# Performance work log

Measured on AMD Instinct MI355X. Metric: run time of the kernel, lower is better.

Reference implementation:

```python
import jax, jax.numpy as jnp
import numpy as np

B, S, D, H, DFF = 2, 2048, 1024, 16, 4096
DK = D // H
EPS = 1e-6

def setup_inputs() -> dict:
    key = jax.random.key(0)
    ks = jax.random.split(key, 12)
    sc = 0.02
    inp = {
        "x": jax.random.normal(ks[0], (B, S, D), jnp.float32),
        "src_mask": jax.random.randint(ks[1], (B, 1, 1, S), 0, 2, jnp.int32),
        "wq": jax.random.normal(ks[2], (D, D), jnp.float32) * sc,
        "bq": jnp.zeros((D,), jnp.float32),
        "wk": jax.random.normal(ks[3], (D, D), jnp.float32) * sc,
        "bk": jnp.zeros((D,), jnp.float32),
        "wv": jax.random.normal(ks[4], (D, D), jnp.float32) * sc,
        "bv": jnp.zeros((D,), jnp.float32),
        "wo": jax.random.normal(ks[5], (D, D), jnp.float32) * sc,
        "bo": jnp.zeros((D,), jnp.float32),
        "w1": jax.random.normal(ks[6], (DFF, D), jnp.float32) * sc,
        "b1": jnp.zeros((DFF,), jnp.float32),
        "w2": jax.random.normal(ks[7], (D, DFF), jnp.float32) * sc,
        "b2": jnp.zeros((D,), jnp.float32),
        "a1": jnp.ones((1,), jnp.float32),
        "be1": jnp.zeros((1,), jnp.float32),
        "a2": jnp.ones((1,), jnp.float32),
        "be2": jnp.zeros((1,), jnp.float32),
    }
    return inp

def layer_norm(x, alpha, beta):
    # custom LN: unbiased std (ddof=1), scalar alpha/beta, divide by (std + eps)
    mean = jnp.mean(x, axis=-1, keepdims=True)
    std = jnp.std(x, axis=-1, keepdims=True, ddof=1)
    return alpha * (x - mean) / (std + EPS) + beta

def mha(x, mask, wq, bq, wk, bk, wv, bv, wo, bo):
    q = (x @ wq.T + bq).reshape(B, S, H, DK).transpose(0, 2, 1, 3)  # [B,H,S,DK]
    k = (x @ wk.T + bk).reshape(B, S, H, DK).transpose(0, 2, 1, 3)
    v = (x @ wv.T + bv).reshape(B, S, H, DK).transpose(0, 2, 1, 3)
    scores = jnp.einsum('bhqd,bhkd->bhqk', q, k) / jnp.sqrt(jnp.float32(DK))
    scores = jnp.where(mask == 0, jnp.float32(-1e9), scores)
    attn = jax.nn.softmax(scores, axis=-1)
    out = jnp.einsum('bhqk,bhkd->bhqd', attn, v)
    out = out.transpose(0, 2, 1, 3).reshape(B, S, D)
    return out @ wo.T + bo

def ffn(x, w1, b1, w2, b2):
    h = jax.nn.relu(x @ w1.T + b1)
    return h @ w2.T + b2

def reference(x, src_mask, wq, bq, wk, bk, wv, bv, wo, bo, w1, b1, w2, b2, a1, be1, a2, be2):
    # pre-norm residual 1: self-attention
    x = x + mha(layer_norm(x, a1, be1), src_mask, wq, bq, wk, bk, wv, bv, wo, bo)
    # pre-norm residual 2: FFN
    x = x + ffn(layer_norm(x, a2, be2), w1, b1, w2, b2)
    return x
```

## Files before the change

### kernel.cpp

```cpp
#include <hip/hip_runtime.h>

#define B_    2
#define S_    2048
#define D_    1024
#define H_    16
#define DK_   64
#define DFF_  4096
#define MROWS (B_*S_)

typedef float f32x4 __attribute__((ext_vector_type(4)));
typedef __bf16 bf16x8 __attribute__((ext_vector_type(8)));

static __device__ __forceinline__ unsigned short f2bf(float f) {
    union { __bf16 h; unsigned short u; } cv;
    cv.h = (__bf16)f;
    return cv.u;
}

static __device__ __forceinline__ void gload16(const unsigned short* g, unsigned short* l) {
    __builtin_amdgcn_global_load_lds((const __attribute__((address_space(1))) void*)g,
                                     (__attribute__((address_space(3))) void*)l, 16, 0, 0);
}

__global__ __launch_bounds__(256) void prep_kernel(
    const float* __restrict__ wq, const float* __restrict__ wk,
    const float* __restrict__ wv, const float* __restrict__ wo,
    const float* __restrict__ w1, const float* __restrict__ w2,
    const float* __restrict__ bq, const float* __restrict__ bk,
    unsigned short* __restrict__ wqkb, unsigned short* __restrict__ wvb,
    unsigned short* __restrict__ wob, unsigned short* __restrict__ w1b,
    unsigned short* __restrict__ w2b, float* __restrict__ bqk) {
    int blk = blockIdx.x;
    if (blk >= 12288) {
        int t0 = threadIdx.x * 8;
        #pragma unroll
        for (int i = 0; i < 8; i++) {
            int j = t0 + i;
            bqk[j] = (j < 1024) ? bq[j] : bk[j - 1024];
        }
        return;
    }
    const float* src; unsigned short* dst; int lb;
    if      (blk < 1024) { src = wq; dst = wqkb;             lb = blk;        }
    else if (blk < 2048) { src = wk; dst = wqkb + (1 << 20); lb = blk - 1024; }
    else if (blk < 3072) { src = wv; dst = wvb;              lb = blk - 2048; }
    else if (blk < 4096) { src = wo; dst = wob;              lb = blk - 3072; }
    else if (blk < 8192) { src = w1; dst = w1b;              lb = blk - 4096; }
    else                 { src = w2; dst = w2b;              lb = blk - 8192; }
    int i4 = lb * 256 + threadIdx.x;
    float4 v = ((const float4*)src)[i4];
    ushort4 o;
    o.x = f2bf(v.x); o.y = f2bf(v.y); o.z = f2bf(v.z); o.w = f2bf(v.w);
    ((ushort4*)dst)[i4] = o;
}

__global__ __launch_bounds__(256) void ln_kernel(const float* __restrict__ x,
                                                 const float* __restrict__ alphap,
                                                 const float* __restrict__ betap,
                                                 unsigned short* __restrict__ out) {
    int row = blockIdx.x;
    int t = threadIdx.x;
    const float* xr = x + (size_t)row * D_;
    float4 v = ((const float4*)xr)[t];
    float s  = v.x + v.y + v.z + v.w;
    float s2 = v.x*v.x + v.y*v.y + v.z*v.z + v.w*v.w;
    #pragma unroll
    for (int o = 1; o < 64; o <<= 1) { s += __shfl_xor(s, o); s2 += __shfl_xor(s2, o); }
    __shared__ float ss[4], ss2[4];
    if ((t & 63) == 0) { ss[t >> 6] = s; ss2[t >> 6] = s2; }
    __syncthreads();
    float S  = ss[0] + ss[1] + ss[2] + ss[3];
    float S2 = ss2[0] + ss2[1] + ss2[2] + ss2[3];
    float mean = S * (1.f / (float)D_);
    float var  = (S2 - S * mean) / (float)(D_ - 1);
    float alpha = alphap[0], beta = betap[0];
    float inv = alpha / (sqrtf(fmaxf(var, 0.f)) + 1e-6f);
    ushort4 o4;
    o4.x = f2bf((v.x - mean) * inv + beta);
    o4.y = f2bf((v.y - mean) * inv + beta);
    o4.z = f2bf((v.z - mean) * inv + beta);
    o4.w = f2bf((v.w - mean) * inv + beta);
    ((ushort4*)(out + (size_t)row * D_))[t] = o4;
}

template<int BN, int EPI, int BIAS_ROW, int QSCALE>
__global__ __launch_bounds__(256) void gemm_bt(const unsigned short* __restrict__ A,
                                               const unsigned short* __restrict__ W,
                                               const float* __restrict__ bias,
                                               const float* __restrict__ resid,
                                               unsigned short* __restrict__ outb,
                                               float* __restrict__ outf,
                                               int M, int N, int K) {
    constexpr int NI = BN / 32;
    __shared__ __align__(16) unsigned short As[128 * 64];
    __shared__ __align__(16) unsigned short Bs[BN * 64];
    const int t = threadIdx.x, lane = t & 63, w = t >> 6;
    const int nwg  = gridDim.x * gridDim.y;
    const int orig = blockIdx.y * gridDim.x + blockIdx.x;
    const int wg   = (orig & 7) * (nwg >> 3) + (orig >> 3);
    const int bx   = wg % gridDim.x, by = wg / gridDim.x;
    const int m0 = by * 128, n0 = bx * BN;
    const int wm = (w & 1) * 64;
    const int wn = (BN == 128) ? (w >> 1) * 64 : (w >> 1) * 32;
    const int l15 = lane & 15, l4 = lane >> 4;
    const int ar0 = w * 8 + (lane >> 3);
    const int ac0 = (lane & 7) * 8;

    f32x4 acc[4][NI];
    f32x4 z4 = {0.f, 0.f, 0.f, 0.f};
    #pragma unroll
    for (int i = 0; i < 4; i++)
        #pragma unroll
        for (int j = 0; j < NI; j++) acc[i][j] = z4;

    const unsigned short* Ap = A + (size_t)m0 * K;
    const unsigned short* Wp = W + (size_t)n0 * K;

    for (int k0 = 0; k0 < K; k0 += 64) {
        #pragma unroll
        for (int j = 0; j < 4; j++)
            gload16(Ap + (size_t)(j*32 + ar0) * K + k0 + ac0, &As[(j*4 + w) * 512]);
        #pragma unroll
        for (int j = 0; j < BN/32; j++)
            gload16(Wp + (size_t)(j*32 + ar0) * K + k0 + ac0, &Bs[(j*4 + w) * 512]);
        __syncthreads();

        #pragma unroll
        for (int ks = 0; ks < 2; ks++) {
            bf16x8 af[4], bfr[NI];
            #pragma unroll
            for (int mi = 0; mi < 4; mi++)
                af[mi] = *(const bf16x8*)&As[(wm + mi*16 + l15)*64 + ks*32 + l4*8];
            #pragma unroll
            for (int ni = 0; ni < NI; ni++)
                bfr[ni] = *(const bf16x8*)&Bs[(wn + ni*16 + l15)*64 + ks*32 + l4*8];
            #pragma unroll
            for (int mi = 0; mi < 4; mi++)
                #pragma unroll
                for (int ni = 0; ni < NI; ni++)
                    acc[mi][ni] = __builtin_amdgcn_mfma_f32_16x16x32_bf16(af[mi], bfr[ni], acc[mi][ni], 0, 0, 0);
        }
        __syncthreads();
    }

    #pragma unroll
    for (int mi = 0; mi < 4; mi++) {
        #pragma unroll
        for (int ni = 0; ni < NI; ni++) {
            int gc = n0 + wn + ni*16 + l15;
            float bc = BIAS_ROW ? 0.f : bias[gc];
            #pragma unroll
            for (int j = 0; j < 4; j++) {
                int gr = m0 + wm + mi*16 + 4*l4 + j;
                float val = acc[mi][ni][j] + (BIAS_ROW ? bias[gr] : bc);
                if (EPI == 1) val = fmaxf(val, 0.f);
                if (QSCALE) { if (gc < (N >> 1)) val *= 0.125f; }
                if (EPI == 2) {
                    val += resid[(size_t)gr * N + gc];
                    outf[(size_t)gr * N + gc] = val;
                } else {
                    outb[(size_t)gr * N + gc] = f2bf(val);
                }
            }
        }
    }
}

__global__ __launch_bounds__(256) void attn_kernel(const unsigned short* __restrict__ qk,
                                                   const unsigned short* __restrict__ vt,
                                                   const int* __restrict__ mask,
                                                   unsigned short* __restrict__ out) {
    __shared__ __align__(16) unsigned short Ks[64*64], Vs[64*64], Ps[64*64];
    __shared__ float mF[64];
    const int t = threadIdx.x, lane = t & 63, w = t >> 6;
    const int l15 = lane & 15, l4 = lane >> 4;
    const int bh = blockIdx.y, b = bh >> 4, h = bh & 15;
    const int q0 = blockIdx.x * 64;
    const unsigned short* qb  = qk + ((size_t)(b * S_ + q0)) * 2048 + h * DK_;
    const unsigned short* kb  = qk + ((size_t)(b * S_)) * 2048 + 1024 + h * DK_;
    const unsigned short* vtb = vt + (size_t)(h * DK_) * MROWS + (size_t)b * S_;

    bf16x8 aq[2];
    #pragma unroll
    for (int ks = 0; ks < 2; ks++)
        aq[ks] = *(const bf16x8*)(qb + (size_t)(w*16 + l15) * 2048 + ks*32 + l4*8);

    float m_ = -INFINITY, l_ = 0.f;
    f32x4 accd[4];
    f32x4 z4 = {0.f, 0.f, 0.f, 0.f};
    #pragma unroll
    for (int dt = 0; dt < 4; dt++) accd[dt] = z4;

    const int r_  = t >> 3, c8_ = (t & 7) * 8;
    const int cs_ = c8_ ^ ((r_ & 7) << 3);
    const int rsw = (l15 & 7) << 3;

    for (int kv0 = 0; kv0 < S_; kv0 += 64) {
        #pragma unroll
        for (int p2 = 0; p2 < 2; p2++) {
            int r = r_ + p2 * 32;
            *(uint4*)&Ks[r*64 + cs_] = *(const uint4*)(kb  + (size_t)(kv0 + r) * 2048 + c8_);
            *(uint4*)&Vs[r*64 + cs_] = *(const uint4*)(vtb + (size_t)r * MROWS + kv0 + c8_);
        }
        if (t < 64) mF[t] = (mask[(size_t)b * S_ + kv0 + t] == 0) ? -1e9f : 0.f;
        __syncthreads();

        f32x4 sc[4];
        #pragma unroll
        for (int nt = 0; nt < 4; nt++) sc[nt] = z4;
        #pragma unroll
        for (int nt = 0; nt < 4; nt++)
            #pragma unroll
            for (int ks = 0; ks < 2; ks++) {
                bf16x8 kf = *(const bf16x8*)&Ks[(nt*16 + l15)*64 + ((ks*32 + 8*l4) ^ rsw)];
                sc[nt] = __builtin_amdgcn_mfma_f32_16x16x32_bf16(kf, aq[ks], sc[nt], 0, 0, 0);
            }

        float sv[4][4];
        #pragma unroll
        for (int nt = 0; nt < 4; nt++) {
            float4 ma = *(const float4*)&mF[nt*16 + 4*l4];
            sv[nt][0] = sc[nt][0] + ma.x;
            sv[nt][1] = sc[nt][1] + ma.y;
            sv[nt][2] = sc[nt][2] + ma.z;
            sv[nt][3] = sc[nt][3] + ma.w;
        }

        float mt = fmaxf(fmaxf(fmaxf(sv[0][0], sv[0][1]), fmaxf(sv[0][2], sv[0][3])),
                         fmaxf(fmaxf(sv[1][0], sv[1][1]), fmaxf(sv[1][2], sv[1][3])));
        mt = fmaxf(mt, fmaxf(fmaxf(fmaxf(sv[2][0], sv[2][1]), fmaxf(sv[2][2], sv[2][3])),
                             fmaxf(fmaxf(sv[3][0], sv[3][1]), fmaxf(sv[3][2], sv[3][3]))));
        mt = fmaxf(mt, __shfl_xor(mt, 16));
        mt = fmaxf(mt, __shfl_xor(mt, 32));

        if (__any(mt > m_)) {
            float mn  = fmaxf(m_, mt);
            float esc = __expf(m_ - mn);
            m_ = mn;
            l_ *= esc;
            float ea[4];
            #pragma unroll
            for (int j = 0; j < 4; j++) ea[j] = __shfl(esc, 4*l4 + j);
            #pragma unroll
            for (int dt = 0; dt < 4; dt++)
                #pragma unroll
                for (int j = 0; j < 4; j++) accd[dt][j] *= ea[j];
        }

        float p[4][4];
        float rsum = 0.f;
        #pragma unroll
        for (int nt = 0; nt < 4; nt++)
            #pragma unroll
            for (int j = 0; j < 4; j++) { p[nt][j] = __expf(sv[nt][j] - m_); rsum += p[nt][j]; }
        rsum += __shfl_xor(rsum, 16);
        rsum += __shfl_xor(rsum, 32);
        l_ += rsum;

        #pragma unroll
        for (int nt = 0; nt < 4; nt++) {
            uint2 w2;
            w2.x = (unsigned)f2bf(p[nt][0]) | ((unsigned)f2bf(p[nt][1]) << 16);
            w2.y = (unsigned)f2bf(p[nt][2]) | ((unsigned)f2bf(p[nt][3]) << 16);
            int key0 = nt*16 + 4*l4;
            *(uint2*)&Ps[(w*16 + l15)*64 + (key0 ^ rsw)] = w2;
        }

        bf16x8 pa[2];
        #pragma unroll
        for (int ks = 0; ks < 2; ks++)
            pa[ks] = *(const bf16x8*)&Ps[(w*16 + l15)*64 + ((ks*32 + 8*l4) ^ rsw)];
        #pragma unroll
        for (int dt = 0; dt < 4; dt++)
            #pragma unroll
            for (int ks = 0; ks < 2; ks++) {
                bf16x8 vv8 = *(const bf16x8*)&Vs[(dt*16 + l15)*64 + ((ks*32 + 8*l4) ^ rsw)];
                accd[dt] = __builtin_amdgcn_mfma_f32_16x16x32_bf16(pa[ks], vv8, accd[dt], 0, 0, 0);
            }
        __syncthreads();
    }

    float inv = 1.f / l_;
    float ia[4];
    #pragma unroll
    for (int j = 0; j < 4; j++) ia[j] = __shfl(inv, 4*l4 + j);
    unsigned short* ob = out + ((size_t)(b * S_ + q0)) * D_ + h * DK_;
    #pragma unroll
    for (int j = 0; j < 4; j++) {
        int r = w*16 + 4*l4 + j;
        #pragma unroll
        for (int dt = 0; dt < 4; dt++)
            ob[(size_t)r * D_ + dt*16 + l15] = f2bf(accd[dt][j] * ia[j]);
    }
}

extern "C" void kernel_launch(void* const* d_in, const int* in_sizes, int n_in,
                              void* d_out, int out_size, void* d_ws, size_t ws_size,
                              hipStream_t stream) {
    const float* x    = (const float*)d_in[0];
    const int*   mask = (const int*)d_in[1];
    const float* wq = (const float*)d_in[2];
    const float* bq = (const float*)d_in[3];
    const float* wk = (const float*)d_in[4];
    const float* bk = (const float*)d_in[5];
    const float* wv = (const float*)d_in[6];
    const float* bv = (const float*)d_in[7];
    const float* wo = (const float*)d_in[8];
    const float* bo = (const float*)d_in[9];
    const float* w1 = (const float*)d_in[10];
    const float* b1 = (const float*)d_in[11];
    const float* w2 = (const float*)d_in[12];
    const float* b2 = (const float*)d_in[13];
    const float* a1  = (const float*)d_in[14];
    const float* be1 = (const float*)d_in[15];
    const float* a2  = (const float*)d_in[16];
    const float* be2 = (const float*)d_in[17];
    float* out = (float*)d_out;

    char* ws = (char*)d_ws;
    unsigned short* wqkb = (unsigned short*)(ws + (0ull  << 20));
    unsigned short* wvb  = (unsigned short*)(ws + (4ull  << 20));
    unsigned short* wob  = (unsigned short*)(ws + (6ull  << 20));
    unsigned short* w1b  = (unsigned short*)(ws + (8ull  << 20));
    unsigned short* w2b  = (unsigned short*)(ws + (16ull << 20));
    unsigned short* xn   = (unsigned short*)(ws + (24ull << 20));
    unsigned short* qkb  = (unsigned short*)(ws + (32ull << 20));
    unsigned short* vtb  = (unsigned short*)(ws + (48ull << 20));
    float*          bqk  = (float*)         (ws + (60ull << 20));
    unsigned short* hh   = qkb;
    float*          x1   = (float*)(ws + (64ull << 20));

    dim3 blk(256);

    prep_kernel<<<12289, blk, 0, stream>>>(wq, wk, wv, wo, w1, w2, bq, bk,
                                           wqkb, wvb, wob, w1b, w2b, bqk);

    ln_kernel<<<MROWS, blk, 0, stream>>>(x, a1, be1, xn);

    dim3 gqk(2048/128, MROWS/128);
    gemm_bt<128,0,0,1><<<gqk, blk, 0, stream>>>(xn, wqkb, bqk, nullptr, qkb, nullptr, MROWS, 2048, D_);

    dim3 gvt(MROWS/64, D_/128);
    gemm_bt<64,0,1,0><<<gvt, blk, 0, stream>>>(wvb, xn, bv, nullptr, vtb, nullptr, D_, MROWS, D_);

    dim3 ga(S_/64, B_*H_);
    attn_kernel<<<ga, blk, 0, stream>>>(qkb, vtb, mask, xn);

    dim3 go(D_/64, MROWS/128);
    gemm_bt<64,2,0,0><<<go, blk, 0, stream>>>(xn, wob, bo, x, nullptr, x1, MROWS, D_, D_);

    ln_kernel<<<MROWS, blk, 0, stream>>>(x1, a2, be2, xn);

    dim3 gf1(DFF_/128, MROWS/128);
    gemm_bt<128,1,0,0><<<gf1, blk, 0, stream>>>(xn, w1b, b1, nullptr, hh, nullptr, MROWS, DFF_, D_);

    gemm_bt<64,2,0,0><<<go, blk, 0, stream>>>(hh, w2b, b2, x1, nullptr, out, MROWS, D_, DFF_);
}
```

Measured before the change: 417.0 us.

## Merge QKV GEMMs, add double-buffered 256x256 FFN1 GEMM, use exp2 softmax

Several changes land together. The QK and V-transposed projections are merged into one launch that splits its blocks between the two GEMMs, which removes one launch and lets the two overlap. FFN1 now runs on a new 256x256-tile, 512-thread GEMM with double-buffered LDS, XOR-swizzled shared memory and setprio around MFMA bursts, which raises data reuse and overlaps the next tile's global loads with compute. The attention softmax switches to exp2 by folding log2(e) into the Q scale (0.125*1.4427). The big tile uses 128KB of LDS, so occupancy drops to one block per CU, and the FFN1 grid is now only 256 workgroups.

```diff
diff --git a/kernel.cpp b/kernel.cpp
--- a/kernel.cpp
+++ b/kernel.cpp
@@ -84,6 +84,83 @@
 }
 
 template<int BN, int EPI, int BIAS_ROW, int QSCALE>
+static __device__ __forceinline__ void gemm_body(unsigned short* As, unsigned short* Bs,
+                                                 const unsigned short* __restrict__ A,
+                                                 const unsigned short* __restrict__ W,
+                                                 const float* __restrict__ bias,
+                                                 const float* __restrict__ resid,
+                                                 unsigned short* __restrict__ outb,
+                                                 float* __restrict__ outf,
+                                                 int M, int N, int K, int bx, int by) {
+    constexpr int NI = BN / 32;
+    const int t = threadIdx.x, lane = t & 63, w = t >> 6;
+    const int m0 = by * 128, n0 = bx * BN;
+    const int wm = (w & 1) * 64;
+    const int wn = (BN == 128) ? (w >> 1) * 64 : (w >> 1) * 32;
+    const int l15 = lane & 15, l4 = lane >> 4;
+    const int ar0 = w * 8 + (lane >> 3);
+    const int ac0 = (lane & 7) * 8;
+
+    f32x4 acc[4][NI];
+    f32x4 z4 = {0.f, 0.f, 0.f, 0.f};
+    #pragma unroll
+    for (int i = 0; i < 4; i++)
+        #pragma unroll
+        for (int j = 0; j < NI; j++) acc[i][j] = z4;
+
+    const unsigned short* Ap = A + (size_t)m0 * K;
+    const unsigned short* Wp = W + (size_t)n0 * K;
+
+    for (int k0 = 0; k0 < K; k0 += 64) {
+        #pragma unroll
+        for (int j = 0; j < 4; j++)
+            gload16(Ap + (size_t)(j*32 + ar0) * K + k0 + ac0, &As[(j*4 + w) * 512]);
+        #pragma unroll
+        for (int j = 0; j < BN/32; j++)
+            gload16(Wp + (size_t)(j*32 + ar0) * K + k0 + ac0, &Bs[(j*4 + w) * 512]);
+        __syncthreads();
+
+        #pragma unroll
+        for (int ks = 0; ks < 2; ks++) {
+            bf16x8 af[4], bfr[NI];
+            #pragma unroll
+            for (int mi = 0; mi < 4; mi++)
+                af[mi] = *(const bf16x8*)&As[(wm + mi*16 + l15)*64 + ks*32 + l4*8];
+            #pragma unroll
+            for (int ni = 0; ni < NI; ni++)
+                bfr[ni] = *(const bf16x8*)&Bs[(wn + ni*16 + l15)*64 + ks*32 + l4*8];
+            #pragma unroll
+            for (int mi = 0; mi < 4; mi++)
+                #pragma unroll
+                for (int ni = 0; ni < NI; ni++)
+                    acc[mi][ni] = __builtin_amdgcn_mfma_f32_16x16x32_bf16(af[mi], bfr[ni], acc[mi][ni], 0, 0, 0);
+        }
+        __syncthreads();
+    }
+
+    #pragma unroll
+    for (int mi = 0; mi < 4; mi++) {
+        #pragma unroll
+        for (int ni = 0; ni < NI; ni++) {
+            int gc = n0 + wn + ni*16 + l15;
+            float bc = BIAS_ROW ? 0.f : bias[gc];
+            #pragma unroll
+            for (int j = 0; j < 4; j++) {
+                int gr = m0 + wm + mi*16 + 4*l4 + j;
+                float val = acc[mi][ni][j] + (BIAS_ROW ? bias[gr] : bc);
+                if (QSCALE) { if (gc < (N >> 1)) val *= 0.180336884f; }
+                if (EPI == 2) {
+                    val += resid[(size_t)gr * N + gc];
+                    outf[(size_t)gr * N + gc] = val;
+                } else {
+                    outb[(size_t)gr * N + gc] = f2bf(val);
+                }
+            }
+        }
+    }
+}
+
+template<int BN, int EPI, int BIAS_ROW, int QSCALE>
 __global__ __launch_bounds__(256) void gemm_bt(const unsigned short* __restrict__ A,
                                                const unsigned short* __restrict__ W,
                                                const float* __restrict__ bias,
@@ -91,76 +168,129 @@
                                                unsigned short* __restrict__ outb,
                                                float* __restrict__ outf,
                                                int M, int N, int K) {
-    constexpr int NI = BN / 32;
     __shared__ __align__(16) unsigned short As[128 * 64];
     __shared__ __align__(16) unsigned short Bs[BN * 64];
-    const int t = threadIdx.x, lane = t & 63, w = t >> 6;
     const int nwg  = gridDim.x * gridDim.y;
     const int orig = blockIdx.y * gridDim.x + blockIdx.x;
     const int wg   = (orig & 7) * (nwg >> 3) + (orig >> 3);
     const int bx   = wg % gridDim.x, by = wg / gridDim.x;
-    const int m0 = by * 128, n0 = bx * BN;
-    const int wm = (w & 1) * 64;
-    const int wn = (BN == 128) ? (w >> 1) * 64 : (w >> 1) * 32;
+    gemm_body<BN,EPI,BIAS_ROW,QSCALE>(As, Bs, A, W, bias, resid, outb, outf, M, N, K, bx, by);
+}
+
+__global__ __launch_bounds__(256) void qkv_kernel(const unsigned short* __restrict__ xn,
+                                                  const unsigned short* __restrict__ wqkb,
+                                                  const float* __restrict__ bqk,
+                                                  const unsigned short* __restrict__ wvb,
+                                                  const float* __restrict__ bv,
+                                                  unsigned short* __restrict__ qkb,
+                                                  unsigned short* __restrict__ vtb) {
+    __shared__ __align__(16) unsigned short As[128 * 64];
+    __shared__ __align__(16) unsigned short Bs[128 * 64];
+    int orig = blockIdx.x;
+    if (orig < 512) {
+        int wg = (orig & 7) * 64 + (orig >> 3);
+        int bx = wg & 15, by = wg >> 4;
+        gemm_body<128,0,0,1>(As, Bs, xn, wqkb, bqk, nullptr, qkb, nullptr, MROWS, 2048, D_, bx, by);
+    } else {
+        int o2 = orig - 512;
+        int wg = (o2 & 7) * 64 + (o2 >> 3);
+        int bx = wg & 63, by = wg >> 6;
+        gemm_body<64,0,1,0>(As, Bs, wvb, xn, bv, nullptr, vtb, nullptr, D_, MROWS, D_, bx, by);
+    }
+}
+
+template<int EPI>
+__global__ __launch_bounds__(512) void gemm256(const unsigned short* __restrict__ A,
+                                               const unsigned short* __restrict__ W,
+                                               const float* __restrict__ bias,
+                                               unsigned short* __restrict__ outb,
+                                               int M, int N, int K) {
+    __shared__ __align__(16) unsigned short Asm[2][256 * 64];
+    __shared__ __align__(16) unsigned short Bsm[2][256 * 64];
+    const int t = threadIdx.x, lane = t & 63, w = t >> 6;
     const int l15 = lane & 15, l4 = lane >> 4;
-    const int ar0 = w * 8 + (lane >> 3);
-    const int ac0 = (lane & 7) * 8;
-
-    f32x4 acc[4][NI];
+    const int nwg  = gridDim.x;
+    const int orig = blockIdx.x;
+    const int wg   = (orig & 7) * (nwg >> 3) + (orig >> 3);
+    const int gx = N >> 8;
+    const int bx = wg % gx, by = wg / gx;
+    const int m0 = by << 8, n0 = bx << 8;
+    const int wr = w >> 2, wc = w & 3;
+    const int srow  = t >> 3;
+    const int sslot = (t & 7) ^ (srow & 7);
+    const unsigned short* Ap = A + (size_t)m0 * K + sslot * 8;
+    const unsigned short* Wp = W + (size_t)n0 * K + sslot * 8;
+    const int ldsb = (w * 8) * 64;
+    const int rsw = (l15 & 7);
+
+    f32x4 acc[8][4];
     f32x4 z4 = {0.f, 0.f, 0.f, 0.f};
     #pragma unroll
-    for (int i = 0; i < 4; i++)
-        #pragma unroll
-        for (int j = 0; j < NI; j++) acc[i][j] = z4;
-
-    const unsigned short* Ap = A + (size_t)m0 * K;
-    const unsigned short* Wp = W + (size_t)n0 * K;
-
-    for (int k0 = 0; k0 < K; k0 += 64) {
-        #pragma unroll
-        for (int j = 0; j < 4; j++)
-            gload16(Ap + (size_t)(j*32 + ar0) * K + k0 + ac0, &As[(j*4 + w) * 512]);
-        #pragma unroll
-        for (int j = 0; j < BN/32; j++)
-            gload16(Wp + (size_t)(j*32 + ar0) * K + k0 + ac0, &Bs[(j*4 + w) * 512]);
-        __syncthreads();
-
-        #pragma unroll
-        for (int ks = 0; ks < 2; ks++) {
-            bf16x8 af[4], bfr[NI];
-            #pragma unroll
-            for (int mi = 0; mi < 4; mi++)
-                af[mi] = *(const bf16x8*)&As[(wm + mi*16 + l15)*64 + ks*32 + l4*8];
-            #pragma unroll
-            for (int ni = 0; ni < NI; ni++)
-                bfr[ni] = *(const bf16x8*)&Bs[(wn + ni*16 + l15)*64 + ks*32 + l4*8];
-            #pragma unroll
-            for (int mi = 0; mi < 4; mi++)
-                #pragma unroll
-                for (int ni = 0; ni < NI; ni++)
-                    acc[mi][ni] = __builtin_amdgcn_mfma_f32_16x16x32_bf16(af[mi], bfr[ni], acc[mi][ni], 0, 0, 0);
-        }
-        __syncthreads();
-    }
-
-    #pragma unroll
-    for (int mi = 0; mi < 4; mi++) {
-        #pragma unroll
-        for (int ni = 0; ni < NI; ni++) {
-            int gc = n0 + wn + ni*16 + l15;
-            float bc = BIAS_ROW ? 0.f : bias[gc];
+    for (int i = 0; i < 8; i++)
+        #pragma unroll
+        for (int j = 0; j < 4; j++) acc[i][j] = z4;
+
+    const int NT = K >> 6;
+    #pragma unroll
+    for (int j = 0; j < 4; j++) gload16(Ap + (size_t)(j*64 + srow) * K, &Asm[0][j*4096 + ldsb]);
+    #pragma unroll
+    for (int j = 0; j < 4; j++) gload16(Wp + (size_t)(j*64 + srow) * K, &Bsm[0][j*4096 + ldsb]);
+
+    for (int T = 0; T < NT; T++) {
+        unsigned short* Ab = Asm[T & 1];
+        unsigned short* Bb = Bsm[T & 1];
+        if (T + 1 < NT) {
+            const size_t k0 = (size_t)(T + 1) << 6;
+            unsigned short* An = Asm[(T + 1) & 1];
+            unsigned short* Bn = Bsm[(T + 1) & 1];
+            #pragma unroll
+            for (int j = 0; j < 4; j++) gload16(Ap + (size_t)(j*64 + srow) * K + k0, &An[j*4096 + ldsb]);
+            #pragma unroll
+            for (int j = 0; j < 4; j++) gload16(Wp + (size_t)(j*64 + srow) * K + k0, &Bn[j*4096 + ldsb]);
+            asm volatile("s_waitcnt vmcnt(8)" ::: "memory");
+        } else {
+            asm volatile("s_waitcnt vmcnt(0)" ::: "memory");
+        }
+        __builtin_amdgcn_sched_barrier(0);
+        __builtin_amdgcn_s_barrier();
+        __builtin_amdgcn_sched_barrier(0);
+
+        bf16x8 af[8][2];
+        #pragma unroll
+        for (int mi = 0; mi < 8; mi++)
+            #pragma unroll
+            for (int kk = 0; kk < 2; kk++)
+                af[mi][kk] = *(const bf16x8*)&Ab[(wr*128 + mi*16 + l15)*64 + (((4*kk + l4) ^ rsw) * 8)];
+        #pragma unroll
+        for (int p = 0; p < 4; p++) {
+            const int brow = (wc*64 + p*16 + l15)*64;
+            bf16x8 bf0 = *(const bf16x8*)&Bb[brow + (((0 + l4) ^ rsw) * 8)];
+            bf16x8 bf1 = *(const bf16x8*)&Bb[brow + (((4 + l4) ^ rsw) * 8)];
+            __builtin_amdgcn_s_setprio(1);
+            #pragma unroll
+            for (int mi = 0; mi < 8; mi++) {
+                acc[mi][p] = __builtin_amdgcn_mfma_f32_16x16x32_bf16(af[mi][0], bf0, acc[mi][p], 0, 0, 0);
+                acc[mi][p] = __builtin_amdgcn_mfma_f32_16x16x32_bf16(af[mi][1], bf1, acc[mi][p], 0, 0, 0);
+            }
+            __builtin_amdgcn_s_setprio(0);
+            __builtin_amdgcn_sched_barrier(0);
+            __builtin_amdgcn_s_barrier();
+            __builtin_amdgcn_sched_barrier(0);
+        }
+    }
+
+    #pragma unroll
+    for (int p = 0; p < 4; p++) {
+        int gc = n0 + wc*64 + p*16 + l15;
+        float bv = bias[gc];
+        #pragma unroll
+        for (int mi = 0; mi < 8; mi++) {
             #pragma unroll
             for (int j = 0; j < 4; j++) {
-                int gr = m0 + wm + mi*16 + 4*l4 + j;
-                float val = acc[mi][ni][j] + (BIAS_ROW ? bias[gr] : bc);
+                int gr = m0 + wr*128 + mi*16 + l4*4 + j;
+                float val = acc[mi][p][j] + bv;
                 if (EPI == 1) val = fmaxf(val, 0.f);
-                if (QSCALE) { if (gc < (N >> 1)) val *= 0.125f; }
-                if (EPI == 2) {
-                    val += resid[(size_t)gr * N + gc];
-                    outf[(size_t)gr * N + gc] = val;
-                } else {
-                    outb[(size_t)gr * N + gc] = f2bf(val);
-                }
+                outb[(size_t)gr * N + gc] = f2bf(val);
             }
         }
     }
@@ -235,7 +365,7 @@
 
         if (__any(mt > m_)) {
             float mn  = fmaxf(m_, mt);
-            float esc = __expf(m_ - mn);
+            float esc = exp2f(m_ - mn);
             m_ = mn;
             l_ *= esc;
             float ea[4];
@@ -252,7 +382,7 @@
         #pragma unroll
         for (int nt = 0; nt < 4; nt++)
             #pragma unroll
-            for (int j = 0; j < 4; j++) { p[nt][j] = __expf(sv[nt][j] - m_); rsum += p[nt][j]; }
+            for (int j = 0; j < 4; j++) { p[nt][j] = exp2f(sv[nt][j] - m_); rsum += p[nt][j]; }
         rsum += __shfl_xor(rsum, 16);
         rsum += __shfl_xor(rsum, 32);
         l_ += rsum;
@@ -337,11 +467,7 @@
 
     ln_kernel<<<MROWS, blk, 0, stream>>>(x, a1, be1, xn);
 
-    dim3 gqk(2048/128, MROWS/128);
-    gemm_bt<128,0,0,1><<<gqk, blk, 0, stream>>>(xn, wqkb, bqk, nullptr, qkb, nullptr, MROWS, 2048, D_);
-
-    dim3 gvt(MROWS/64, D_/128);
-    gemm_bt<64,0,1,0><<<gvt, blk, 0, stream>>>(wvb, xn, bv, nullptr, vtb, nullptr, D_, MROWS, D_);
+    qkv_kernel<<<1024, blk, 0, stream>>>(xn, wqkb, bqk, wvb, bv, qkb, vtb);
 
     dim3 ga(S_/64, B_*H_);
     attn_kernel<<<ga, blk, 0, stream>>>(qkb, vtb, mask, xn);
@@ -351,8 +477,7 @@
 
     ln_kernel<<<MROWS, blk, 0, stream>>>(x1, a2, be2, xn);
 
-    dim3 gf1(DFF_/128, MROWS/128);
-    gemm_bt<128,1,0,0><<<gf1, blk, 0, stream>>>(xn, w1b, b1, nullptr, hh, nullptr, MROWS, DFF_, D_);
+    gemm256<1><<<256, 512, 0, stream>>>(xn, w1b, b1, hh, MROWS, DFF_, D_);
 
     gemm_bt<64,2,0,0><<<go, blk, 0, stream>>>(hh, w2b, b2, x1, nullptr, out, MROWS, D_, DFF_);
 }
```

Measured after the change: 412.7 us. Within noise of the previous version (-1.0%).
